# Kernel tuning notes

Measured on AMD Instinct MI355X. Metric: run time of the kernel, lower is better.

## Reference

```python
import jax, jax.numpy as jnp
import numpy as np

# HT config: input_shape = output_shape = (8,8,8,8), rank = 8, d = 4 modes
B = 4096
M = 8      # per-mode input dim
N = 8      # per-mode output dim
R = 8      # HT rank
FEAT = M ** 4  # 4096


def setup_inputs() -> dict:
    key = jax.random.key(0)
    ks = jax.random.split(key, 8)
    x = jax.random.normal(ks[0], (B, FEAT), dtype=jnp.float32)
    # leaf factors: (in_p, out_p, rank); xavier-style scale over the input mode
    f_std = np.float32(np.sqrt(2.0 / (M + N * R)))
    F0 = jax.random.normal(ks[1], (M, N, R), dtype=jnp.float32) * f_std
    F1 = jax.random.normal(ks[2], (M, N, R), dtype=jnp.float32) * f_std
    F2 = jax.random.normal(ks[3], (M, N, R), dtype=jnp.float32) * f_std
    F3 = jax.random.normal(ks[4], (M, N, R), dtype=jnp.float32) * f_std
    # internal cores: (left_rank, right_rank, parent_rank)
    c_std = np.float32(np.sqrt(2.0 / (R + R * R)))
    CL = jax.random.normal(ks[5], (R, R, R), dtype=jnp.float32) * c_std
    CR = jax.random.normal(ks[6], (R, R, R), dtype=jnp.float32) * c_std
    bound = np.float32(1.0 / np.sqrt(FEAT))
    bias = jax.random.uniform(ks[7], (FEAT,), dtype=jnp.float32, minval=-bound, maxval=bound)
    return {"x": x, "F0": F0, "F1": F1, "F2": F2, "F3": F3,
            "CL": CL, "CR": CR, "bias": bias}


def reference(x, F0, F1, F2, F3, CL, CR, bias):
    b = x.shape[0]
    # (b, i, j, k, l): one axis per HT mode
    x4 = x.reshape(b, M, M, M, M)
    # Pre-contract each subtree's two leaves with its core (tiny tensors):
    # left transfer  W_L[i, j, a, c, p], right transfer W_R[k, l, d, e, p].
    # This is the same tensor-network contraction as the tn.Node graph,
    # just in an efficient associativity order.
    WL = jnp.einsum('iar,jcs,rsp->ijacp', F0, F1, CL)
    WR = jnp.einsum('kdr,les,rsp->kldep', F2, F3, CR)
    # contract left subtree against the input: (b, k, l, a, c, p)
    yL = jnp.einsum('bijkl,ijacp->bklacp', x4, WL)
    # contract right subtree; parent edges of the two subtrees are joined (p)
    y = jnp.einsum('bklacp,kldep->bacde', yL, WR)
    return y.reshape(b, FEAT) + bias
```

## Files before the change

### kernel.cpp

```cpp
#include <hip/hip_runtime.h>
#include <hip/hip_bf16.h>


typedef short bf16x8 __attribute__((ext_vector_type(8)));
typedef float f32x4  __attribute__((ext_vector_type(4)));

union Frag8 {
    bf16x8 v;
    unsigned int u4[4];
    uint2 u2[2];
};

static __device__ __forceinline__ unsigned int pkbf(float a, float b) {
    __hip_bfloat162 h = __float22bfloat162_rn(float2{a, b});
    return *reinterpret_cast<unsigned int*>(&h);
}

static __device__ __forceinline__ unsigned short f2bf(float f) {
    unsigned int u = __float_as_uint(f);
    u = (u + 0x7FFFu + ((u >> 16) & 1u)) >> 16;
    return (unsigned short)u;
}

__global__ void ht_precompute(const float* __restrict__ F0, const float* __restrict__ F1,
                              const float* __restrict__ F2, const float* __restrict__ F3,
                              const float* __restrict__ CL, const float* __restrict__ CR,
                              unsigned short* __restrict__ frags) {
    int idx = blockIdx.x * blockDim.x + threadIdx.x;
    int isW = idx >> 15;
    int r15 = idx & 32767;
    int p    = r15 >> 12;
    int f    = (r15 >> 9) & 7;
    int lane = (r15 >> 3) & 63;
    int j    = r15 & 7;
    int cb = f >> 1, ks = f & 1;
    int n = cb * 16 + (lane & 15);
    int k = ks * 32 + ((lane >> 4) & 3) * 8 + j;
    const float* Fa = isW ? F2 : F0;
    const float* Fb = isW ? F3 : F1;
    const float* C  = isW ? CR : CL;
    int i1 = k >> 3, i2 = k & 7, o1 = n >> 3, o2 = n & 7;
    float acc = 0.f;
    for (int r = 0; r < 8; ++r) {
        float fa = Fa[(i1 * 8 + o1) * 8 + r];
        for (int s = 0; s < 8; ++s)
            acc += fa * Fb[(i2 * 8 + o2) * 8 + s] * C[(r * 8 + s) * 8 + p];
    }
    frags[(size_t)isW * 32768 + ((p * 8 + f) << 9) + lane * 8 + j] = f2bf(acc);
}

#define T_PITCH 68

__global__ __launch_bounds__(256) void ht_main(const float* __restrict__ x,
                                               const unsigned short* __restrict__ frags,
                                               const float* __restrict__ bias,
                                               float* __restrict__ out) {
    __shared__ unsigned short Tl[4 * 64 * T_PITCH];
    const int tid  = threadIdx.x;
    const int lane = tid & 63;
    const int w    = __builtin_amdgcn_readfirstlane(tid >> 6);
    const int b    = blockIdx.x * 4 + w;
    unsigned short* Tw = Tl + w * (64 * T_PITCH);

    const int l15 = lane & 15;
    const int q   = lane >> 4;

    Frag8 xf[4][2];
    const float* xb = x + ((size_t)b << 12);
#pragma unroll
    for (int rb = 0; rb < 4; ++rb)
#pragma unroll
        for (int ks = 0; ks < 2; ++ks) {
            const float* src = xb + (ks * 32 + q * 8) * 64 + rb * 16 + l15;
#pragma unroll
            for (int j = 0; j < 8; j += 2)
                xf[rb][ks].u4[j >> 1] = pkbf(src[j * 64], src[(j + 1) * 64]);
        }

    f32x4 acc[4][4];
#pragma unroll
    for (int i = 0; i < 4; ++i)
#pragma unroll
        for (int j = 0; j < 4; ++j)
            acc[i][j] = f32x4{0.f, 0.f, 0.f, 0.f};

    const unsigned short* AF = frags;
    const unsigned short* WF = frags + 32768;

#pragma unroll 1
    for (int p = 0; p < 8; ++p) {
        Frag8 af[4][2];
#pragma unroll
        for (int cb = 0; cb < 4; ++cb)
#pragma unroll
            for (int ks = 0; ks < 2; ++ks)
                af[cb][ks].v = *(const bf16x8*)(AF + (((p * 8 + cb * 2 + ks) << 9) + lane * 8));
#pragma unroll
        for (int rb = 0; rb < 4; ++rb) {
#pragma unroll
            for (int cb = 0; cb < 4; ++cb) {
                f32x4 t = f32x4{0.f, 0.f, 0.f, 0.f};
                t = __builtin_amdgcn_mfma_f32_16x16x32_bf16(xf[rb][0].v, af[cb][0].v, t, 0, 0, 0);
                t = __builtin_amdgcn_mfma_f32_16x16x32_bf16(xf[rb][1].v, af[cb][1].v, t, 0, 0, 0);
                int ac = cb * 16 + l15;
                int kl = rb * 16 + q * 4;
                uint2 wv;
                wv.x = pkbf(t[0], t[1]);
                wv.y = pkbf(t[2], t[3]);
                *(uint2*)(&Tw[ac * T_PITCH + kl]) = wv;
            }
        }
        Frag8 wf[4][2];
#pragma unroll
        for (int cb = 0; cb < 4; ++cb)
#pragma unroll
            for (int ks = 0; ks < 2; ++ks)
                wf[cb][ks].v = *(const bf16x8*)(WF + (((p * 8 + cb * 2 + ks) << 9) + lane * 8));
        Frag8 tf[4][2];
#pragma unroll
        for (int rb = 0; rb < 4; ++rb)
#pragma unroll
            for (int ks = 0; ks < 2; ++ks) {
                int ac = rb * 16 + l15;
                int kl = ks * 32 + q * 8;
                tf[rb][ks].u2[0] = *(const uint2*)(&Tw[ac * T_PITCH + kl]);
                tf[rb][ks].u2[1] = *(const uint2*)(&Tw[ac * T_PITCH + kl + 4]);
            }
#pragma unroll
        for (int rb = 0; rb < 4; ++rb)
#pragma unroll
            for (int cb = 0; cb < 4; ++cb) {
                acc[rb][cb] = __builtin_amdgcn_mfma_f32_16x16x32_bf16(tf[rb][0].v, wf[cb][0].v, acc[rb][cb], 0, 0, 0);
                acc[rb][cb] = __builtin_amdgcn_mfma_f32_16x16x32_bf16(tf[rb][1].v, wf[cb][1].v, acc[rb][cb], 0, 0, 0);
            }
    }

    float* ob = out + ((size_t)b << 12);
#pragma unroll
    for (int rb = 0; rb < 4; ++rb)
#pragma unroll
        for (int cb = 0; cb < 4; ++cb) {
            int de  = cb * 16 + l15;
            int ac0 = rb * 16 + q * 4;
#pragma unroll
            for (int r = 0; r < 4; ++r) {
                int o = (ac0 + r) * 64 + de;
                ob[o] = acc[rb][cb][r] + bias[o];
            }
        }
}

extern "C" void kernel_launch(void* const* d_in, const int* in_sizes, int n_in,
                              void* d_out, int out_size, void* d_ws, size_t ws_size,
                              hipStream_t stream) {
    const float* x    = (const float*)d_in[0];
    const float* F0   = (const float*)d_in[1];
    const float* F1   = (const float*)d_in[2];
    const float* F2   = (const float*)d_in[3];
    const float* F3   = (const float*)d_in[4];
    const float* CL   = (const float*)d_in[5];
    const float* CR   = (const float*)d_in[6];
    const float* bias = (const float*)d_in[7];
    float* out = (float*)d_out;
    unsigned short* frags = (unsigned short*)d_ws;

    const int B = in_sizes[0] / 4096;

    ht_precompute<<<256, 256, 0, stream>>>(F0, F1, F2, F3, CL, CR, frags);
    ht_main<<<B / 4, 256, 0, stream>>>(x, frags, bias, out);
}
```

Before: 150.0 us.

## Software-pipeline first-stage MFMA for next rank slice with second-stage contraction

New measurement: 211.9 us. 1.41x slower.

```diff
diff --git a/kernel.cpp b/kernel.cpp
--- a/kernel.cpp
+++ b/kernel.cpp
@@ -87,35 +87,32 @@
     const unsigned short* AF = frags;
     const unsigned short* WF = frags + 32768;
 
-#pragma unroll 1
-    for (int p = 0; p < 8; ++p) {
+    const int wr_ac = l15;
+    const int wr_kl = q * 4;
+
+    {
         Frag8 af[4][2];
 #pragma unroll
         for (int cb = 0; cb < 4; ++cb)
 #pragma unroll
             for (int ks = 0; ks < 2; ++ks)
-                af[cb][ks].v = *(const bf16x8*)(AF + (((p * 8 + cb * 2 + ks) << 9) + lane * 8));
+                af[cb][ks].v = *(const bf16x8*)(AF + (((0 * 8 + cb * 2 + ks) << 9) + lane * 8));
 #pragma unroll
-        for (int rb = 0; rb < 4; ++rb) {
+        for (int rb = 0; rb < 4; ++rb)
 #pragma unroll
             for (int cb = 0; cb < 4; ++cb) {
                 f32x4 t = f32x4{0.f, 0.f, 0.f, 0.f};
                 t = __builtin_amdgcn_mfma_f32_16x16x32_bf16(xf[rb][0].v, af[cb][0].v, t, 0, 0, 0);
                 t = __builtin_amdgcn_mfma_f32_16x16x32_bf16(xf[rb][1].v, af[cb][1].v, t, 0, 0, 0);
-                int ac = cb * 16 + l15;
-                int kl = rb * 16 + q * 4;
                 uint2 wv;
                 wv.x = pkbf(t[0], t[1]);
                 wv.y = pkbf(t[2], t[3]);
-                *(uint2*)(&Tw[ac * T_PITCH + kl]) = wv;
+                *(uint2*)(&Tw[(cb * 16 + wr_ac) * T_PITCH + rb * 16 + wr_kl]) = wv;
             }
-        }
-        Frag8 wf[4][2];
+    }
+
 #pragma unroll
-        for (int cb = 0; cb < 4; ++cb)
-#pragma unroll
-            for (int ks = 0; ks < 2; ++ks)
-                wf[cb][ks].v = *(const bf16x8*)(WF + (((p * 8 + cb * 2 + ks) << 9) + lane * 8));
+    for (int p = 0; p < 8; ++p) {
         Frag8 tf[4][2];
 #pragma unroll
         for (int rb = 0; rb < 4; ++rb)
@@ -126,6 +123,32 @@
                 tf[rb][ks].u2[0] = *(const uint2*)(&Tw[ac * T_PITCH + kl]);
                 tf[rb][ks].u2[1] = *(const uint2*)(&Tw[ac * T_PITCH + kl + 4]);
             }
+        Frag8 wf[4][2];
+#pragma unroll
+        for (int cb = 0; cb < 4; ++cb)
+#pragma unroll
+            for (int ks = 0; ks < 2; ++ks)
+                wf[cb][ks].v = *(const bf16x8*)(WF + (((p * 8 + cb * 2 + ks) << 9) + lane * 8));
+        if (p < 7) {
+            Frag8 af[4][2];
+#pragma unroll
+            for (int cb = 0; cb < 4; ++cb)
+#pragma unroll
+                for (int ks = 0; ks < 2; ++ks)
+                    af[cb][ks].v = *(const bf16x8*)(AF + ((((p + 1) * 8 + cb * 2 + ks) << 9) + lane * 8));
+#pragma unroll
+            for (int rb = 0; rb < 4; ++rb)
+#pragma unroll
+                for (int cb = 0; cb < 4; ++cb) {
+                    f32x4 t = f32x4{0.f, 0.f, 0.f, 0.f};
+                    t = __builtin_amdgcn_mfma_f32_16x16x32_bf16(xf[rb][0].v, af[cb][0].v, t, 0, 0, 0);
+                    t = __builtin_amdgcn_mfma_f32_16x16x32_bf16(xf[rb][1].v, af[cb][1].v, t, 0, 0, 0);
+                    uint2 wv;
+                    wv.x = pkbf(t[0], t[1]);
+                    wv.y = pkbf(t[2], t[3]);
+                    *(uint2*)(&Tw[(cb * 16 + wr_ac) * T_PITCH + rb * 16 + wr_kl]) = wv;
+                }
+        }
 #pragma unroll
         for (int rb = 0; rb < 4; ++rb)
 #pragma unroll
```

## Switch HT contraction to 32x32x16 bf16 MFMA tiles with occupancy hint

Applied to the files above, without the earlier changes.

New measurement: 227.0 us. 51.4% more time.

```diff
diff --git a/kernel.cpp b/kernel.cpp
--- a/kernel.cpp
+++ b/kernel.cpp
@@ -2,8 +2,8 @@
 #include <hip/hip_bf16.h>
 
 
-typedef short bf16x8 __attribute__((ext_vector_type(8)));
-typedef float f32x4  __attribute__((ext_vector_type(4)));
+typedef short  bf16x8 __attribute__((ext_vector_type(8)));
+typedef float  f32x16 __attribute__((ext_vector_type(16)));
 
 union Frag8 {
     bf16x8 v;
@@ -28,14 +28,13 @@
                               unsigned short* __restrict__ frags) {
     int idx = blockIdx.x * blockDim.x + threadIdx.x;
     int isW = idx >> 15;
-    int r15 = idx & 32767;
-    int p    = r15 >> 12;
-    int f    = (r15 >> 9) & 7;
-    int lane = (r15 >> 3) & 63;
-    int j    = r15 & 7;
-    int cb = f >> 1, ks = f & 1;
-    int n = cb * 16 + (lane & 15);
-    int k = ks * 32 + ((lane >> 4) & 3) * 8 + j;
+    int p    = (idx >> 12) & 7;
+    int f    = (idx >> 9) & 7;
+    int lane = (idx >> 3) & 63;
+    int j    = idx & 7;
+    int nb = f >> 2, kk = f & 3;
+    int n = nb * 32 + (lane & 31);
+    int k = kk * 16 + ((lane >> 5) & 1) * 8 + j;
     const float* Fa = isW ? F2 : F0;
     const float* Fb = isW ? F3 : F1;
     const float* C  = isW ? CR : CL;
@@ -51,10 +50,10 @@
 
 #define T_PITCH 68
 
-__global__ __launch_bounds__(256) void ht_main(const float* __restrict__ x,
-                                               const unsigned short* __restrict__ frags,
-                                               const float* __restrict__ bias,
-                                               float* __restrict__ out) {
+__global__ __launch_bounds__(256, 4) void ht_main(const float* __restrict__ x,
+                                                  const unsigned short* __restrict__ frags,
+                                                  const float* __restrict__ bias,
+                                                  float* __restrict__ out) {
     __shared__ unsigned short Tl[4 * 64 * T_PITCH];
     const int tid  = threadIdx.x;
     const int lane = tid & 63;
@@ -62,91 +61,94 @@
     const int b    = blockIdx.x * 4 + w;
     unsigned short* Tw = Tl + w * (64 * T_PITCH);
 
-    const int l15 = lane & 15;
-    const int q   = lane >> 4;
+    const int l31 = lane & 31;
+    const int h   = (lane >> 5) & 1;
 
-    Frag8 xf[4][2];
+    Frag8 xf[2][4];
     const float* xb = x + ((size_t)b << 12);
 #pragma unroll
-    for (int rb = 0; rb < 4; ++rb)
+    for (int mb = 0; mb < 2; ++mb)
 #pragma unroll
-        for (int ks = 0; ks < 2; ++ks) {
-            const float* src = xb + (ks * 32 + q * 8) * 64 + rb * 16 + l15;
+        for (int kk = 0; kk < 4; ++kk) {
+            const float* src = xb + (kk * 16 + h * 8) * 64 + mb * 32 + l31;
 #pragma unroll
             for (int j = 0; j < 8; j += 2)
-                xf[rb][ks].u4[j >> 1] = pkbf(src[j * 64], src[(j + 1) * 64]);
+                xf[mb][kk].u4[j >> 1] = pkbf(src[j * 64], src[(j + 1) * 64]);
         }
 
-    f32x4 acc[4][4];
+    f32x16 acc[2][2];
 #pragma unroll
-    for (int i = 0; i < 4; ++i)
+    for (int i = 0; i < 2; ++i)
 #pragma unroll
-        for (int j = 0; j < 4; ++j)
-            acc[i][j] = f32x4{0.f, 0.f, 0.f, 0.f};
+        for (int j = 0; j < 2; ++j)
+#pragma unroll
+            for (int e = 0; e < 16; ++e)
+                acc[i][j][e] = 0.f;
 
     const unsigned short* AF = frags;
     const unsigned short* WF = frags + 32768;
 
 #pragma unroll 1
     for (int p = 0; p < 8; ++p) {
-        Frag8 af[4][2];
 #pragma unroll
-        for (int cb = 0; cb < 4; ++cb)
+        for (int nb = 0; nb < 2; ++nb) {
+            Frag8 af[4];
 #pragma unroll
-            for (int ks = 0; ks < 2; ++ks)
-                af[cb][ks].v = *(const bf16x8*)(AF + (((p * 8 + cb * 2 + ks) << 9) + lane * 8));
+            for (int kk = 0; kk < 4; ++kk)
+                af[kk].v = *(const bf16x8*)(AF + (((p * 8 + nb * 4 + kk) << 9) + lane * 8));
 #pragma unroll
-        for (int rb = 0; rb < 4; ++rb) {
+            for (int mb = 0; mb < 2; ++mb) {
+                f32x16 t;
 #pragma unroll
-            for (int cb = 0; cb < 4; ++cb) {
-                f32x4 t = f32x4{0.f, 0.f, 0.f, 0.f};
-                t = __builtin_amdgcn_mfma_f32_16x16x32_bf16(xf[rb][0].v, af[cb][0].v, t, 0, 0, 0);
-                t = __builtin_amdgcn_mfma_f32_16x16x32_bf16(xf[rb][1].v, af[cb][1].v, t, 0, 0, 0);
-                int ac = cb * 16 + l15;
-                int kl = rb * 16 + q * 4;
-                uint2 wv;
-                wv.x = pkbf(t[0], t[1]);
-                wv.y = pkbf(t[2], t[3]);
-                *(uint2*)(&Tw[ac * T_PITCH + kl]) = wv;
+                for (int e = 0; e < 16; ++e) t[e] = 0.f;
+#pragma unroll
+                for (int kk = 0; kk < 4; ++kk)
+                    t = __builtin_amdgcn_mfma_f32_32x32x16_bf16(xf[mb][kk].v, af[kk].v, t, 0, 0, 0);
+#pragma unroll
+                for (int g = 0; g < 4; ++g) {
+                    uint2 wv;
+                    wv.x = pkbf(t[4 * g + 0], t[4 * g + 1]);
+                    wv.y = pkbf(t[4 * g + 2], t[4 * g + 3]);
+                    *(uint2*)(&Tw[(nb * 32 + l31) * T_PITCH + mb * 32 + 8 * g + 4 * h]) = wv;
+                }
             }
         }
-        Frag8 wf[4][2];
 #pragma unroll
-        for (int cb = 0; cb < 4; ++cb)
+        for (int nb = 0; nb < 2; ++nb) {
+            Frag8 wfr[4];
 #pragma unroll
-            for (int ks = 0; ks < 2; ++ks)
-                wf[cb][ks].v = *(const bf16x8*)(WF + (((p * 8 + cb * 2 + ks) << 9) + lane * 8));
-        Frag8 tf[4][2];
+            for (int kk = 0; kk < 4; ++kk)
+                wfr[kk].v = *(const bf16x8*)(WF + (((p * 8 + nb * 4 + kk) << 9) + lane * 8));
 #pragma unroll
-        for (int rb = 0; rb < 4; ++rb)
+            for (int rb = 0; rb < 2; ++rb) {
+                Frag8 tf[4];
 #pragma unroll
-            for (int ks = 0; ks < 2; ++ks) {
-                int ac = rb * 16 + l15;
-                int kl = ks * 32 + q * 8;
-                tf[rb][ks].u2[0] = *(const uint2*)(&Tw[ac * T_PITCH + kl]);
-                tf[rb][ks].u2[1] = *(const uint2*)(&Tw[ac * T_PITCH + kl + 4]);
+                for (int kk = 0; kk < 4; ++kk) {
+                    const unsigned short* src = &Tw[(rb * 32 + l31) * T_PITCH + kk * 16 + h * 8];
+                    tf[kk].u2[0] = *(const uint2*)(src);
+                    tf[kk].u2[1] = *(const uint2*)(src + 4);
+                }
+#pragma unroll
+                for (int kk = 0; kk < 4; ++kk)
+                    acc[rb][nb] = __builtin_amdgcn_mfma_f32_32x32x16_bf16(tf[kk].v, wfr[kk].v, acc[rb][nb], 0, 0, 0);
             }
-#pragma unroll
-        for (int rb = 0; rb < 4; ++rb)
-#pragma unroll
-            for (int cb = 0; cb < 4; ++cb) {
-                acc[rb][cb] = __builtin_amdgcn_mfma_f32_16x16x32_bf16(tf[rb][0].v, wf[cb][0].v, acc[rb][cb], 0, 0, 0);
-                acc[rb][cb] = __builtin_amdgcn_mfma_f32_16x16x32_bf16(tf[rb][1].v, wf[cb][1].v, acc[rb][cb], 0, 0, 0);
-            }
+        }
     }
 
     float* ob = out + ((size_t)b << 12);
 #pragma unroll
-    for (int rb = 0; rb < 4; ++rb)
+    for (int rb = 0; rb < 2; ++rb)
 #pragma unroll
-        for (int cb = 0; cb < 4; ++cb) {
-            int de  = cb * 16 + l15;
-            int ac0 = rb * 16 + q * 4;
+        for (int nb = 0; nb < 2; ++nb) {
+            int de = nb * 32 + l31;
 #pragma unroll
-            for (int r = 0; r < 4; ++r) {
-                int o = (ac0 + r) * 64 + de;
-                ob[o] = acc[rb][cb][r] + bias[o];
-            }
+            for (int g = 0; g < 4; ++g)
+#pragma unroll
+                for (int r = 0; r < 4; ++r) {
+                    int ac = rb * 32 + 8 * g + 4 * h + r;
+                    int o  = ac * 64 + de;
+                    ob[o] = acc[rb][nb][4 * g + r] + bias[o];
+                }
         }
 }
 
```
